# Optimization experiments

Hardware: AMD Instinct MI355X
Metric: run time of the kernel (lower is better)

Reference implementation:

```python
import jax, jax.numpy as jnp
import numpy as np

TEMPERATURE = 0.5
EPSILON = 1e-08
NEG_POS_RATIO = 4
B = 4096          # per-view batch
D = 512           # embedding dim
N = 2 * B         # total rows in sim matrix


def setup_inputs() -> dict:
    key = jax.random.key(0)
    k1, k2, k3 = jax.random.split(key, 3)
    z_i = jax.random.normal(k1, (B, D), dtype=jnp.float32)
    z_j = jax.random.normal(k2, (B, D), dtype=jnp.float32)
    # torch.multinomial over uniform ones, with replacement, over the 2B-1
    # non-diagonal columns == uniform randint in [0, N-1).
    neg_idx = jax.random.randint(k3, (N, NEG_POS_RATIO), 0, N - 1, dtype=jnp.int32)
    return {"z_i": z_i, "z_j": z_j, "neg_idx": neg_idx}


def reference(z_i, z_j, neg_idx):
    z = jnp.concatenate((z_i, z_j), axis=0)                      # [N, D]
    # cosine similarity matrix via normalize + matmul (same math as
    # F.cosine_similarity(z[:,None], z[None,:], dim=2), eps=1e-8 default)
    zn = z / jnp.maximum(jnp.linalg.norm(z, axis=1, keepdims=True), 1e-8)
    sim = (zn @ zn.T) / (TEMPERATURE + EPSILON)                  # [N, N]

    rows = jnp.arange(N)
    positives = sim[rows, (rows + B) % N]                        # [N]

    # negatives_all[i] = sim[i] with column i removed; sampled index k in
    # [0, N-1) maps to original column k if k < i else k + 1.
    cols = neg_idx + (neg_idx >= rows[:, None]).astype(neg_idx.dtype)  # [N, R]
    negatives = jnp.take_along_axis(sim, cols, axis=1)           # [N, R]

    logits = jnp.concatenate((positives[:, None], negatives), axis=1)  # [N, 1+R]
    nll = -jax.nn.log_softmax(logits, axis=1)[:, 0]              # labels all 0
    # weighted CE with weight[0]=neg_pos_ratio; all labels are 0 so the
    # per-sample weight cancels in the mean reduction:
    # loss = sum(w0 * nll) / sum(w0) = mean(nll)
    w0 = jnp.float32(NEG_POS_RATIO)
    loss = (w0 * nll).sum() / (w0 * N)
    return loss
```

## Files before the change

kernel.cpp:

```cpp
#include <hip/hip_runtime.h>
#include <math.h>

#define B_ROWS 4096
#define D_DIM  512
#define N_ROWS 8192
#define R_NEG  4
#define NBLOCKS (N_ROWS / 4)

#define INV_T 2.0f

__device__ __forceinline__ float dot4(float4 a, float4 b) {
  return a.x * b.x + a.y * b.y + a.z * b.z + a.w * b.w;
}

__global__ __launch_bounds__(256) void fused_loss_kernel(
    const float* __restrict__ zi, const float* __restrict__ zj,
    const int* __restrict__ neg_idx, float* __restrict__ partials) {
  __shared__ float s_nll[4];

  const int wave = threadIdx.x >> 6;
  const int lane = threadIdx.x & 63;
  const int row  = blockIdx.x * 4 + wave;

  const int4 nv = ((const int4*)neg_idx)[row];
  int cols[5];
  cols[0] = (row + B_ROWS) & (N_ROWS - 1);
  cols[1] = nv.x + (nv.x >= row ? 1 : 0);
  cols[2] = nv.y + (nv.y >= row ? 1 : 0);
  cols[3] = nv.z + (nv.z >= row ? 1 : 0);
  cols[4] = nv.w + (nv.w >= row ? 1 : 0);

  const float4* a4 =
      (row < B_ROWS) ? (const float4*)(zi + (size_t)row * D_DIM)
                     : (const float4*)(zj + (size_t)(row - B_ROWS) * D_DIM);
  float4 a0 = a4[lane];
  float4 a1 = a4[lane + 64];

  float4 b0[5], b1[5];
#pragma unroll
  for (int c = 0; c < 5; ++c) {
    const int col = cols[c];
    const float4* b4 =
        (col < B_ROWS) ? (const float4*)(zi + (size_t)col * D_DIM)
                       : (const float4*)(zj + (size_t)(col - B_ROWS) * D_DIM);
    b0[c] = b4[lane];
    b1[c] = b4[lane + 64];
  }

  float aa = dot4(a0, a0) + dot4(a1, a1);
  float ab[5], bb[5];
#pragma unroll
  for (int c = 0; c < 5; ++c) {
    ab[c] = dot4(a0, b0[c]) + dot4(a1, b1[c]);
    bb[c] = dot4(b0[c], b0[c]) + dot4(b1[c], b1[c]);
  }

#pragma unroll
  for (int off = 32; off > 0; off >>= 1) {
    aa += __shfl_down(aa, off);
#pragma unroll
    for (int c = 0; c < 5; ++c) {
      ab[c] += __shfl_down(ab[c], off);
      bb[c] += __shfl_down(bb[c], off);
    }
  }

  if (lane == 0) {
    const float inv_a = 1.0f / fmaxf(sqrtf(aa), 1e-8f);
    float logits[5];
    float m = -INFINITY;
#pragma unroll
    for (int c = 0; c < 5; ++c) {
      const float inv_b = 1.0f / fmaxf(sqrtf(bb[c]), 1e-8f);
      logits[c] = ab[c] * inv_a * inv_b * INV_T;
      m = fmaxf(m, logits[c]);
    }
    float sum = 0.0f;
#pragma unroll
    for (int c = 0; c < 5; ++c) sum += __expf(logits[c] - m);
    s_nll[wave] = -(logits[0] - m - __logf(sum));
  }
  __syncthreads();

  if (threadIdx.x == 0) {
    partials[blockIdx.x] = s_nll[0] + s_nll[1] + s_nll[2] + s_nll[3];
  }
}

__global__ __launch_bounds__(256) void reduce_kernel(
    const float* __restrict__ partials, float* __restrict__ out) {
  __shared__ float smem[4];
  const int lane = threadIdx.x & 63;
  const int wave = threadIdx.x >> 6;
  float s = 0.0f;
#pragma unroll
  for (int i = 0; i < NBLOCKS / 256; ++i) s += partials[i * 256 + threadIdx.x];
#pragma unroll
  for (int off = 32; off > 0; off >>= 1) s += __shfl_down(s, off);
  if (lane == 0) smem[wave] = s;
  __syncthreads();
  if (threadIdx.x == 0) {
    out[0] = (smem[0] + smem[1] + smem[2] + smem[3]) * (1.0f / (float)N_ROWS);
  }
}

extern "C" void kernel_launch(void* const* d_in, const int* in_sizes, int n_in,
                              void* d_out, int out_size, void* d_ws,
                              size_t ws_size, hipStream_t stream) {
  const float* zi      = (const float*)d_in[0];
  const float* zj      = (const float*)d_in[1];
  const int*   neg_idx = (const int*)d_in[2];
  float* out = (float*)d_out;
  float* partials = (float*)d_ws;

  fused_loss_kernel<<<dim3(NBLOCKS), dim3(256), 0, stream>>>(
      zi, zj, neg_idx, partials);
  reduce_kernel<<<dim3(1), dim3(256), 0, stream>>>(partials, out);
}
```

Before: 78.97 us.

## Precompute inverse row norms in separate kernel and split dot products across waves

Adds a norm_kernel that computes the inverse L2 norm of every row once, so the loss kernel no longer recomputes norms for the positive and sampled negative columns. Each row's dot products are now split across two waves, with halves of D combined through shared memory, which doubles the loss grid to raise parallelism. In exchange it adds a third kernel launch and an extra pass over all of z. The loss kernel still reads the five gathered rows, so total memory traffic may grow.

After: 82.78 us. 1.05x slower.

```diff
diff --git a/kernel.cpp b/kernel.cpp
--- a/kernel.cpp
+++ b/kernel.cpp
@@ -5,22 +5,48 @@
 #define D_DIM  512
 #define N_ROWS 8192
 #define R_NEG  4
-#define NBLOCKS (N_ROWS / 4)
 
 #define INV_T 2.0f
+
+#define NORM_BLOCKS (N_ROWS / 4)
+#define LOSS_BLOCKS (N_ROWS / 2)
+#define RED_ITERS   (LOSS_BLOCKS / 256)
+
 
 __device__ __forceinline__ float dot4(float4 a, float4 b) {
   return a.x * b.x + a.y * b.y + a.z * b.z + a.w * b.w;
 }
 
-__global__ __launch_bounds__(256) void fused_loss_kernel(
+__global__ __launch_bounds__(256, 8) void norm_kernel(
     const float* __restrict__ zi, const float* __restrict__ zj,
-    const int* __restrict__ neg_idx, float* __restrict__ partials) {
-  __shared__ float s_nll[4];
+    float* __restrict__ invn) {
+  const int wave = threadIdx.x >> 6;
+  const int lane = threadIdx.x & 63;
+  const int row  = blockIdx.x * 4 + wave;
+
+  const float4* a4 =
+      (row < B_ROWS) ? (const float4*)(zi + (size_t)row * D_DIM)
+                     : (const float4*)(zj + (size_t)(row - B_ROWS) * D_DIM);
+  float4 a0 = a4[lane];
+  float4 a1 = a4[lane + 64];
+  float aa = dot4(a0, a0) + dot4(a1, a1);
+#pragma unroll
+  for (int off = 32; off > 0; off >>= 1) aa += __shfl_down(aa, off);
+  if (lane == 0) invn[row] = 1.0f / fmaxf(sqrtf(aa), 1e-8f);
+}
+
+__global__ __launch_bounds__(256, 8) void loss_kernel(
+    const float* __restrict__ zi, const float* __restrict__ zj,
+    const int* __restrict__ neg_idx, const float* __restrict__ invn,
+    float* __restrict__ partials) {
+  __shared__ float s_ab[4][5];
+  __shared__ float s_nll[2];
 
   const int wave = threadIdx.x >> 6;
   const int lane = threadIdx.x & 63;
-  const int row  = blockIdx.x * 4 + wave;
+  const int rloc = wave >> 1;
+  const int half = wave & 1;
+  const int row  = blockIdx.x * 2 + rloc;
 
   const int4 nv = ((const int4*)neg_idx)[row];
   int cols[5];
@@ -30,60 +56,62 @@
   cols[3] = nv.z + (nv.z >= row ? 1 : 0);
   cols[4] = nv.w + (nv.w >= row ? 1 : 0);
 
+  const float inv_r = invn[row];
+  float invc[5];
+#pragma unroll
+  for (int c = 0; c < 5; ++c) invc[c] = invn[cols[c]];
+
+  const int off = lane + half * 64;
+
   const float4* a4 =
       (row < B_ROWS) ? (const float4*)(zi + (size_t)row * D_DIM)
                      : (const float4*)(zj + (size_t)(row - B_ROWS) * D_DIM);
-  float4 a0 = a4[lane];
-  float4 a1 = a4[lane + 64];
+  float4 a = a4[off];
 
-  float4 b0[5], b1[5];
+  float4 b[5];
 #pragma unroll
   for (int c = 0; c < 5; ++c) {
     const int col = cols[c];
     const float4* b4 =
         (col < B_ROWS) ? (const float4*)(zi + (size_t)col * D_DIM)
                        : (const float4*)(zj + (size_t)(col - B_ROWS) * D_DIM);
-    b0[c] = b4[lane];
-    b1[c] = b4[lane + 64];
+    b[c] = b4[off];
   }
 
-  float aa = dot4(a0, a0) + dot4(a1, a1);
-  float ab[5], bb[5];
+  float ab[5];
 #pragma unroll
-  for (int c = 0; c < 5; ++c) {
-    ab[c] = dot4(a0, b0[c]) + dot4(a1, b1[c]);
-    bb[c] = dot4(b0[c], b0[c]) + dot4(b1[c], b1[c]);
-  }
+  for (int c = 0; c < 5; ++c) ab[c] = dot4(a, b[c]);
 
 #pragma unroll
-  for (int off = 32; off > 0; off >>= 1) {
-    aa += __shfl_down(aa, off);
+  for (int o = 32; o > 0; o >>= 1) {
 #pragma unroll
-    for (int c = 0; c < 5; ++c) {
-      ab[c] += __shfl_down(ab[c], off);
-      bb[c] += __shfl_down(bb[c], off);
-    }
+    for (int c = 0; c < 5; ++c) ab[c] += __shfl_down(ab[c], o);
   }
 
   if (lane == 0) {
-    const float inv_a = 1.0f / fmaxf(sqrtf(aa), 1e-8f);
+#pragma unroll
+    for (int c = 0; c < 5; ++c) s_ab[wave][c] = ab[c];
+  }
+  __syncthreads();
+
+  if (lane == 0 && half == 0) {
     float logits[5];
     float m = -INFINITY;
 #pragma unroll
     for (int c = 0; c < 5; ++c) {
-      const float inv_b = 1.0f / fmaxf(sqrtf(bb[c]), 1e-8f);
-      logits[c] = ab[c] * inv_a * inv_b * INV_T;
+      const float abf = s_ab[wave][c] + s_ab[wave + 1][c];
+      logits[c] = abf * inv_r * invc[c] * INV_T;
       m = fmaxf(m, logits[c]);
     }
     float sum = 0.0f;
 #pragma unroll
     for (int c = 0; c < 5; ++c) sum += __expf(logits[c] - m);
-    s_nll[wave] = -(logits[0] - m - __logf(sum));
+    s_nll[rloc] = -(logits[0] - m - __logf(sum));
   }
   __syncthreads();
 
   if (threadIdx.x == 0) {
-    partials[blockIdx.x] = s_nll[0] + s_nll[1] + s_nll[2] + s_nll[3];
+    partials[blockIdx.x] = s_nll[0] + s_nll[1];
   }
 }
 
@@ -94,7 +122,7 @@
   const int wave = threadIdx.x >> 6;
   float s = 0.0f;
 #pragma unroll
-  for (int i = 0; i < NBLOCKS / 256; ++i) s += partials[i * 256 + threadIdx.x];
+  for (int i = 0; i < RED_ITERS; ++i) s += partials[i * 256 + threadIdx.x];
 #pragma unroll
   for (int off = 32; off > 0; off >>= 1) s += __shfl_down(s, off);
   if (lane == 0) smem[wave] = s;
@@ -111,9 +139,12 @@
   const float* zj      = (const float*)d_in[1];
   const int*   neg_idx = (const int*)d_in[2];
   float* out = (float*)d_out;
-  float* partials = (float*)d_ws;
 
-  fused_loss_kernel<<<dim3(NBLOCKS), dim3(256), 0, stream>>>(
-      zi, zj, neg_idx, partials);
+  float* invn     = (float*)d_ws;
+  float* partials = invn + N_ROWS;
+
+  norm_kernel<<<dim3(NORM_BLOCKS), dim3(256), 0, stream>>>(zi, zj, invn);
+  loss_kernel<<<dim3(LOSS_BLOCKS), dim3(256), 0, stream>>>(zi, zj, neg_idx,
+                                                           invn, partials);
   reduce_kernel<<<dim3(1), dim3(256), 0, stream>>>(partials, out);
 }
```

## Precompute normalized fp16 rows, then gather half-precision rows in loss kernel

Applied to the files above, without the earlier changes.

Adds a pre-pass that normalizes each embedding row once and stores it as fp16 in workspace. The loss kernel then gathers the anchor, positive and negative rows in fp16 and only computes dot products, with no per-column norms. The aim is to halve the bytes gathered and remove norm work that was repeated for every sampled column. In exchange it adds a kernel launch, an 8 MB intermediate write, and fp16 rounding of the similarities.

After: 77.26 us. 2.2% less time.

```diff
diff --git a/kernel.cpp b/kernel.cpp
--- a/kernel.cpp
+++ b/kernel.cpp
@@ -1,21 +1,66 @@
 #include <hip/hip_runtime.h>
+#include <hip/hip_fp16.h>
 #include <math.h>
 
 #define B_ROWS 4096
 #define D_DIM  512
 #define N_ROWS 8192
 #define R_NEG  4
-#define NBLOCKS (N_ROWS / 4)
 
 #define INV_T 2.0f
+
+#define NORM_BLOCKS (N_ROWS / 4)
+#define LOSS_BLOCKS (N_ROWS / 4)
+#define RED_ITERS   (LOSS_BLOCKS / 256)
+
 
 __device__ __forceinline__ float dot4(float4 a, float4 b) {
   return a.x * b.x + a.y * b.y + a.z * b.z + a.w * b.w;
 }
 
-__global__ __launch_bounds__(256) void fused_loss_kernel(
+__device__ __forceinline__ float dot8h(uint4 a, uint4 b) {
+  const __half2* ah = (const __half2*)&a;
+  const __half2* bh = (const __half2*)&b;
+  float s = 0.0f;
+#pragma unroll
+  for (int k = 0; k < 4; ++k) {
+    float2 af = __half22float2(ah[k]);
+    float2 bf = __half22float2(bh[k]);
+    s += af.x * bf.x + af.y * bf.y;
+  }
+  return s;
+}
+
+__global__ __launch_bounds__(256, 8) void norm_kernel(
     const float* __restrict__ zi, const float* __restrict__ zj,
-    const int* __restrict__ neg_idx, float* __restrict__ partials) {
+    __half* __restrict__ zh) {
+  const int wave = threadIdx.x >> 6;
+  const int lane = threadIdx.x & 63;
+  const int row  = blockIdx.x * 4 + wave;
+
+  const float4* a4 =
+      (row < B_ROWS) ? (const float4*)(zi + (size_t)row * D_DIM)
+                     : (const float4*)(zj + (size_t)(row - B_ROWS) * D_DIM);
+  float4 a0 = a4[lane];
+  float4 a1 = a4[lane + 64];
+  float aa = dot4(a0, a0) + dot4(a1, a1);
+#pragma unroll
+  for (int off = 32; off > 0; off >>= 1) aa += __shfl_xor(aa, off);
+  const float inv = 1.0f / fmaxf(sqrtf(aa), 1e-8f);
+
+  uint2* out = (uint2*)(zh + (size_t)row * D_DIM);
+  union { uint2 u; __half2 h[2]; } p0, p1;
+  p0.h[0] = __floats2half2_rn(a0.x * inv, a0.y * inv);
+  p0.h[1] = __floats2half2_rn(a0.z * inv, a0.w * inv);
+  p1.h[0] = __floats2half2_rn(a1.x * inv, a1.y * inv);
+  p1.h[1] = __floats2half2_rn(a1.z * inv, a1.w * inv);
+  out[lane]      = p0.u;
+  out[lane + 64] = p1.u;
+}
+
+__global__ __launch_bounds__(256, 8) void loss_kernel(
+    const __half* __restrict__ zh, const int* __restrict__ neg_idx,
+    float* __restrict__ partials) {
   __shared__ float s_nll[4];
 
   const int wave = threadIdx.x >> 6;
@@ -30,49 +75,31 @@
   cols[3] = nv.z + (nv.z >= row ? 1 : 0);
   cols[4] = nv.w + (nv.w >= row ? 1 : 0);
 
-  const float4* a4 =
-      (row < B_ROWS) ? (const float4*)(zi + (size_t)row * D_DIM)
-                     : (const float4*)(zj + (size_t)(row - B_ROWS) * D_DIM);
-  float4 a0 = a4[lane];
-  float4 a1 = a4[lane + 64];
+  const uint4* a4 = (const uint4*)(zh + (size_t)row * D_DIM);
+  uint4 a = a4[lane];
 
-  float4 b0[5], b1[5];
+  uint4 b[5];
 #pragma unroll
   for (int c = 0; c < 5; ++c) {
-    const int col = cols[c];
-    const float4* b4 =
-        (col < B_ROWS) ? (const float4*)(zi + (size_t)col * D_DIM)
-                       : (const float4*)(zj + (size_t)(col - B_ROWS) * D_DIM);
-    b0[c] = b4[lane];
-    b1[c] = b4[lane + 64];
+    b[c] = ((const uint4*)(zh + (size_t)cols[c] * D_DIM))[lane];
   }
 
-  float aa = dot4(a0, a0) + dot4(a1, a1);
-  float ab[5], bb[5];
+  float ab[5];
 #pragma unroll
-  for (int c = 0; c < 5; ++c) {
-    ab[c] = dot4(a0, b0[c]) + dot4(a1, b1[c]);
-    bb[c] = dot4(b0[c], b0[c]) + dot4(b1[c], b1[c]);
-  }
+  for (int c = 0; c < 5; ++c) ab[c] = dot8h(a, b[c]);
 
 #pragma unroll
-  for (int off = 32; off > 0; off >>= 1) {
-    aa += __shfl_down(aa, off);
+  for (int o = 32; o > 0; o >>= 1) {
 #pragma unroll
-    for (int c = 0; c < 5; ++c) {
-      ab[c] += __shfl_down(ab[c], off);
-      bb[c] += __shfl_down(bb[c], off);
-    }
+    for (int c = 0; c < 5; ++c) ab[c] += __shfl_down(ab[c], o);
   }
 
   if (lane == 0) {
-    const float inv_a = 1.0f / fmaxf(sqrtf(aa), 1e-8f);
     float logits[5];
     float m = -INFINITY;
 #pragma unroll
     for (int c = 0; c < 5; ++c) {
-      const float inv_b = 1.0f / fmaxf(sqrtf(bb[c]), 1e-8f);
-      logits[c] = ab[c] * inv_a * inv_b * INV_T;
+      logits[c] = ab[c] * INV_T;
       m = fmaxf(m, logits[c]);
     }
     float sum = 0.0f;
@@ -94,7 +121,7 @@
   const int wave = threadIdx.x >> 6;
   float s = 0.0f;
 #pragma unroll
-  for (int i = 0; i < NBLOCKS / 256; ++i) s += partials[i * 256 + threadIdx.x];
+  for (int i = 0; i < RED_ITERS; ++i) s += partials[i * 256 + threadIdx.x];
 #pragma unroll
   for (int off = 32; off > 0; off >>= 1) s += __shfl_down(s, off);
   if (lane == 0) smem[wave] = s;
@@ -111,9 +138,13 @@
   const float* zj      = (const float*)d_in[1];
   const int*   neg_idx = (const int*)d_in[2];
   float* out = (float*)d_out;
-  float* partials = (float*)d_ws;
 
-  fused_loss_kernel<<<dim3(NBLOCKS), dim3(256), 0, stream>>>(
-      zi, zj, neg_idx, partials);
+  char* w = (char*)d_ws;
+  __half* zh      = (__half*)w;
+  float*  partials = (float*)(w + (size_t)N_ROWS * D_DIM * sizeof(__half));
+
+  norm_kernel<<<dim3(NORM_BLOCKS), dim3(256), 0, stream>>>(zi, zj, zh);
+  loss_kernel<<<dim3(LOSS_BLOCKS), dim3(256), 0, stream>>>(zh, neg_idx,
+                                                           partials);
   reduce_kernel<<<dim3(1), dim3(256), 0, stream>>>(partials, out);
 }
```
